# Kernel optimization log

Measured on AMD Instinct MI355X. Metric: run time of the kernel, lower is better.

## Reference

```python
import jax, jax.numpy as jnp
import numpy as np

B, S, D, H = 2, 2048, 1024, 16
DK = D // H


def setup_inputs() -> dict:
    key = jax.random.key(0)
    ks = jax.random.split(key, 8)
    s = 1.0 / np.sqrt(D)
    return {
        "query": jax.random.normal(ks[0], (B, S, D), jnp.float32),
        "key": jax.random.normal(ks[1], (B, S, D), jnp.float32),
        "value": jax.random.normal(ks[2], (B, S, D), jnp.float32),
        "mask": jnp.ones((B, S), jnp.int32),
        "w_q": jax.random.normal(ks[3], (D, D), jnp.float32) * s,
        "w_k": jax.random.normal(ks[4], (D, D), jnp.float32) * s,
        "w_v": jax.random.normal(ks[5], (D, D), jnp.float32) * s,
        "w_o": jax.random.normal(ks[6], (D, D), jnp.float32) * s,
        "b_o": jnp.zeros((D,), jnp.float32),
    }


def reference(query, key, value, mask, w_q, w_k, w_v, w_o, b_o):
    scale = np.sqrt(DK).astype(np.float32)
    # Linear layers: torch stores weight as [out, in], y = x @ W.T
    Q = (query @ w_q.T).reshape(B, S, H, DK).transpose(0, 2, 1, 3)  # [B,H,S,DK]
    K = (key @ w_k.T).reshape(B, S, H, DK).transpose(0, 2, 1, 3)
    V = (value @ w_v.T).reshape(B, S, H, DK).transpose(0, 2, 1, 3)
    scores = jnp.einsum("bhqd,bhkd->bhqk", Q, K) / scale  # [B,H,S,S]
    m = mask[:, None, None, :]  # [B,1,1,S]
    scores = jnp.where(m == 0, jnp.float32(-1e9), scores)
    attn = jax.nn.softmax(scores, axis=-1)  # dropout in eval mode = identity
    ctx = jnp.einsum("bhqk,bhkd->bhqd", attn, V)
    ctx = ctx.transpose(0, 2, 1, 3).reshape(B, S, D)
    out = ctx @ w_o.T + b_o
    return out, attn
```

## Files before the change

### kernel.cpp

```cpp
#include <hip/hip_runtime.h>
#include <hip/hip_bf16.h>
#include <math.h>

#define B 2
#define S 2048
#define D 1024
#define H 16
#define DK 64

typedef __attribute__((ext_vector_type(8))) short bf8;
typedef __attribute__((ext_vector_type(8))) unsigned short u16x8;
typedef __attribute__((ext_vector_type(4))) unsigned short u16x4;
typedef __attribute__((ext_vector_type(4))) float f32x4;
typedef unsigned short ush;

__device__ __forceinline__ float bf2f(ush u) {
    union { unsigned int i; float f; } v; v.i = ((unsigned int)u) << 16; return v.f;
}
__device__ __forceinline__ ush f2bf_rne(float x) {
    __hip_bfloat16 h = __float2bfloat16(x);
    union { __hip_bfloat16 h; ush u; } v; v.h = h; return v.u;
}
__device__ __forceinline__ ush f2bf_trunc(float x) {
    union { float f; unsigned int i; } v; v.f = x; return (ush)(v.i >> 16);
}

__device__ __forceinline__ void gl16(const void* g, void* l) {
    __builtin_amdgcn_global_load_lds(
        (const __attribute__((address_space(1))) void*)g,
        (__attribute__((address_space(3))) void*)l, 16, 0, 0);
}

#define FENCE()    asm volatile("" ::: "memory")
#define WAIT_VM(N) asm volatile("s_waitcnt vmcnt(" #N ")" ::: "memory")
#define BARRAW()   __builtin_amdgcn_s_barrier()

__global__ __launch_bounds__(256) void conv_hex_k(
    const float* __restrict__ q,  ush* __restrict__ qh,  ush* __restrict__ qlo,
    const float* __restrict__ wq, ush* __restrict__ wqh, ush* __restrict__ wql,
    const float* __restrict__ k,  ush* __restrict__ kh,  ush* __restrict__ klo,
    const float* __restrict__ wk, ush* __restrict__ wkh, ush* __restrict__ wkl,
    const float* __restrict__ v,  ush* __restrict__ vh,
    const float* __restrict__ wv, ush* __restrict__ wvh,
    int nbX, int nbW)
{
    int bx = blockIdx.x;
    const float* src; ush* oh; ush* ol;
    if (bx < nbX) { src = q; oh = qh; ol = qlo; }
    else { bx -= nbX;
      if (bx < nbW) { src = wq; oh = wqh; ol = wql; }
      else { bx -= nbW;
        if (bx < nbX) { src = k; oh = kh; ol = klo; }
        else { bx -= nbX;
          if (bx < nbW) { src = wk; oh = wkh; ol = wkl; }
          else { bx -= nbW;
            if (bx < nbX) { src = v; oh = vh; ol = nullptr; }
            else { bx -= nbX; src = wv; oh = wvh; ol = nullptr; }
          } } } }
    const size_t t = (size_t)bx * 256 + threadIdx.x;

    const float4* s4 = (const float4*)src + t * 2;
    float4 a = s4[0], c = s4[1];
    float vv[8] = {a.x, a.y, a.z, a.w, c.x, c.y, c.z, c.w};
    u16x8 hi;
#pragma unroll
    for (int j = 0; j < 8; ++j) hi[j] = f2bf_trunc(vv[j]);
    *(u16x8*)&oh[t * 8] = hi;
    if (ol) {
        u16x8 lo;
#pragma unroll
        for (int j = 0; j < 8; ++j) lo[j] = f2bf_rne(vv[j] - bf2f(hi[j]));
        *(u16x8*)&ol[t * 8] = lo;
    }
}

__global__ __launch_bounds__(256) void conv_hi_k(
    const float* __restrict__ X, ush* __restrict__ Oh)
{
    const size_t t = (size_t)blockIdx.x * 256 + threadIdx.x;
    const float4* s4 = (const float4*)X + t * 2;
    float4 a = s4[0], c = s4[1];
    float v[8] = {a.x, a.y, a.z, a.w, c.x, c.y, c.z, c.w};
    u16x8 hi;
#pragma unroll
    for (int j = 0; j < 8; ++j) hi[j] = f2bf_trunc(v[j]);
    *(u16x8*)&Oh[t * 8] = hi;
}

template<bool SPLIT, int EPI>
__device__ __forceinline__ void gemm_body2(
    const ush* __restrict__ Xh, const ush* __restrict__ Xl,
    const ush* __restrict__ Wh, const ush* __restrict__ Wl,
    const float* __restrict__ bias, void* __restrict__ Y0v, void* __restrict__ Y1v,
    ush* BufS)
{
    const int tid  = threadIdx.x;
    const int lane = tid & 63;
    const int w    = tid >> 6;
    const int wn   = w >> 1, wm = w & 1;
    const int m0   = blockIdx.x * 64;
    const int n0   = blockIdx.y * 128;

    f32x4 acc[4][2];
#pragma unroll
    for (int s = 0; s < 4; ++s)
#pragma unroll
        for (int t = 0; t < 2; ++t) acc[s][t] = (f32x4){0.f, 0.f, 0.f, 0.f};

    const int kg = (lane >> 4) * 8;
    const int rb = lane >> 3;
    const int jd = lane & 7;
    const int kS = SPLIT ? 32 : 16;

    auto stage = [&](ush* buf, int ks) {
#pragma unroll
        for (int i = 0; i < 6; ++i) {
            int rd = w * 48 + i * 8 + rb;
            int jo = jd ^ (rd & 7);
            const ush* src;
            if (rd < 128) {
                if (SPLIT)
                    src = (jo < 4) ? Xh + (size_t)(n0 + rd) * 1024 + ks * 32 + jo * 8
                                   : Xl + (size_t)(n0 + rd) * 1024 + ks * 32 + (jo - 4) * 8;
                else
                    src = Xh + (size_t)(n0 + rd) * 1024 + ks * 64 + jo * 8;
            } else {
                int rw = rd - 128;
                if (SPLIT)
                    src = (jo < 4) ? Wh + (size_t)(m0 + rw) * 1024 + ks * 32 + jo * 8
                                   : Wl + (size_t)(m0 + rw) * 1024 + ks * 32 + (jo - 4) * 8;
                else
                    src = Wh + (size_t)(m0 + rw) * 1024 + ks * 64 + jo * 8;
            }
            gl16(src, &buf[(w * 48 + i * 8) * 64]);
        }
    };

    auto step = [&](const ush* buf) {
        bf8 a0[4], a1[4], b0[2], b1[2];
#pragma unroll
        for (int s = 0; s < 4; ++s) {
            int r = wn * 64 + s * 16 + (lane & 15);
            a0[s] = *(const bf8*)&buf[r * 64 + (kg ^ ((r & 7) << 3))];
            a1[s] = *(const bf8*)&buf[r * 64 + ((32 + kg) ^ ((r & 7) << 3))];
        }
#pragma unroll
        for (int t = 0; t < 2; ++t) {
            int r = wm * 32 + t * 16 + (lane & 15);
            b0[t] = *(const bf8*)&buf[(128 + r) * 64 + (kg ^ ((r & 7) << 3))];
            b1[t] = *(const bf8*)&buf[(128 + r) * 64 + ((32 + kg) ^ ((r & 7) << 3))];
        }
#pragma unroll
        for (int s = 0; s < 4; ++s)
#pragma unroll
            for (int t = 0; t < 2; ++t) {
                acc[s][t] = __builtin_amdgcn_mfma_f32_16x16x32_bf16(a0[s], b0[t], acc[s][t], 0, 0, 0);
                if (SPLIT) {
                    acc[s][t] = __builtin_amdgcn_mfma_f32_16x16x32_bf16(a0[s], b1[t], acc[s][t], 0, 0, 0);
                    acc[s][t] = __builtin_amdgcn_mfma_f32_16x16x32_bf16(a1[s], b0[t], acc[s][t], 0, 0, 0);
                } else {
                    acc[s][t] = __builtin_amdgcn_mfma_f32_16x16x32_bf16(a1[s], b1[t], acc[s][t], 0, 0, 0);
                }
            }
    };

    stage(&BufS[0 * 12288], 0);
    stage(&BufS[1 * 12288], 1);
    FENCE();
    WAIT_VM(6); BARRAW(); FENCE();

    for (int kt = 0; kt < kS; ++kt) {
        const int pf = kt + 2;
        if (pf < kS) { stage(&BufS[(pf % 3) * 12288], pf); FENCE(); }
        step(&BufS[(kt % 3) * 12288]);
        if (kt + 2 < kS)      { WAIT_VM(6); }
        else if (kt + 1 < kS) { WAIT_VM(0); }
        BARRAW(); FENCE();
    }

#pragma unroll
    for (int s = 0; s < 4; ++s)
#pragma unroll
        for (int t = 0; t < 2; ++t) {
            const int nb = n0 + wn * 64 + 16 * s + 4 * (lane >> 4);
            const int m  = m0 + wm * 32 + 16 * t + (lane & 15);
            if (EPI == 0) {
                float* Y = (float*)Y0v;
                const float bb = bias[m];
#pragma unroll
                for (int r = 0; r < 4; ++r)
                    __builtin_nontemporal_store(acc[s][t][r] + bb,
                                                &Y[(size_t)(nb + r) * 1024 + m]);
            } else if (EPI == 1) {
                ush* Yh = (ush*)Y0v;
                ush* Yl = (ush*)Y1v;
#pragma unroll
                for (int r = 0; r < 4; ++r) {
                    float v = acc[s][t][r];
                    ush hi = f2bf_trunc(v);
                    Yh[(size_t)(nb + r) * 1024 + m] = hi;
                    Yl[(size_t)(nb + r) * 1024 + m] = f2bf_rne(v - bf2f(hi));
                }
            } else {
                ush* Vt = (ush*)Y0v;
                u16x4 pk;
#pragma unroll
                for (int r = 0; r < 4; ++r) pk[r] = f2bf_rne(acc[s][t][r]);
                size_t addr = ((size_t)(nb >> 11) * 1024 + m) * 2048 + (nb & 2047);
                *(u16x4*)&Vt[addr] = pk;
            }
        }
}

__global__ __launch_bounds__(256) void gemm_proj3(
    const ush* __restrict__ qXh, const ush* __restrict__ qXl,
    const ush* __restrict__ wqH, const ush* __restrict__ wqL,
    ush* __restrict__ Qh, ush* __restrict__ Ql,
    const ush* __restrict__ kXh, const ush* __restrict__ kXl,
    const ush* __restrict__ wkH, const ush* __restrict__ wkL,
    ush* __restrict__ Kh, ush* __restrict__ Kl,
    const ush* __restrict__ vXh, const ush* __restrict__ wvH,
    ush* __restrict__ Vt)
{
    __shared__ __align__(16) ush BufS[3 * 192 * 64];
    const int z = blockIdx.z;
    if (z == 0)      gemm_body2<true, 1>(qXh, qXl, wqH, wqL, nullptr, Qh, Ql, BufS);
    else if (z == 1) gemm_body2<true, 1>(kXh, kXl, wkH, wkL, nullptr, Kh, Kl, BufS);
    else             gemm_body2<false, 2>(vXh, nullptr, wvH, nullptr, nullptr, Vt, nullptr, BufS);
}

__global__ __launch_bounds__(256) void gemm_outk(
    const ush* __restrict__ Xh, const ush* __restrict__ Wh,
    const float* __restrict__ bias, float* __restrict__ Y)
{
    __shared__ __align__(16) ush BufS[3 * 192 * 64];
    gemm_body2<false, 0>(Xh, nullptr, Wh, nullptr, bias, Y, nullptr, BufS);
}

__global__ __launch_bounds__(512) void attn_mfma4(
    const ush* __restrict__ Qh, const ush* __restrict__ Ql,
    const ush* __restrict__ Kh, const ush* __restrict__ Kl,
    const ush* __restrict__ Vt, const int* __restrict__ maskg,
    float* __restrict__ attn, ush* __restrict__ ctx)
{
    const int tid  = threadIdx.x;
    const int lane = tid & 63;
    const int w    = tid >> 6;
    const int lid  = blockIdx.x + (blockIdx.y << 4) + (blockIdx.z << 8);
    const int swz  = ((lid & 7) << 6) | (lid >> 3);
    const int qt = swz & 15, h = (swz >> 4) & 15, b = swz >> 8;
    const int q0 = qt * 128;

    __shared__ __align__(16) ush KhsD[3][4096];
    __shared__ __align__(16) ush KlsD[2][4096];
    __shared__ __align__(16) ush VtsD[2][4096];
    __shared__ __align__(16) ush Pus[8][1024];
    __shared__ float biasS[2048];

    const int kg = (lane >> 4) * 8;
    const int q  = lane & 15;
    const int qrow = q0 + w * 16 + q;
    const int rb = lane >> 3;
    const int jd = lane & 7;

    const ush* KhT = Kh + (size_t)(b * S) * 1024 + h * DK;
    const ush* KlT = Kl + (size_t)(b * S) * 1024 + h * DK;
    const ush* VtT = Vt + (size_t)(b * 1024 + h * DK) * 2048;

    {
        const int t4 = tid * 4;
        int4 mv = *(const int4*)&maskg[b * S + t4];
        biasS[t4 + 0] = mv.x ? 0.f : -1e9f;
        biasS[t4 + 1] = mv.y ? 0.f : -1e9f;
        biasS[t4 + 2] = mv.z ? 0.f : -1e9f;
        biasS[t4 + 3] = mv.w ? 0.f : -1e9f;
    }

    bf8 qh[2], ql[2];
    {
        const ush* p1 = Qh + (size_t)(b * S + qrow) * D + h * DK + kg;
        qh[0] = *(const bf8*)p1; qh[1] = *(const bf8*)(p1 + 32);
        const ush* p2 = Ql + (size_t)(b * S + qrow) * D + h * DK + kg;
        ql[0] = *(const bf8*)p2; ql[1] = *(const bf8*)(p2 + 32);
    }

    const int rd = w * 8 + rb;
    const int jo = jd ^ (rd & 7);

    auto stKh = [&](int bufi, int k0) {
        gl16(KhT + (size_t)(k0 + rd) * 1024 + jo * 8, &KhsD[bufi][(w * 8) * 64]);
    };
    auto stKl = [&](int bufi, int k0) {
        gl16(KlT + (size_t)(k0 + rd) * 1024 + jo * 8, &KlsD[bufi][(w * 8) * 64]);
    };
    auto stVt = [&](int bufi, int k0) {
        gl16(VtT + (size_t)rd * 2048 + k0 + jo * 8, &VtsD[bufi][(w * 8) * 64]);
    };

    const float scale = 0.125f;
    float mrow = -1e30f, lrow = 0.f;

    auto computeA = [&](const ush* Khs_, int k0) {
        f32x4 sacc[4];
#pragma unroll
        for (int st = 0; st < 4; ++st) sacc[st] = (f32x4){0.f, 0.f, 0.f, 0.f};
#pragma unroll
        for (int st = 0; st < 4; ++st) {
            int r = st * 16 + q;
#pragma unroll
            for (int dh = 0; dh < 2; ++dh) {
                bf8 kf = *(const bf8*)&Khs_[r * 64 + ((dh * 32 + kg) ^ ((r & 7) << 3))];
                sacc[st] = __builtin_amdgcn_mfma_f32_16x16x32_bf16(kf, qh[dh], sacc[st], 0, 0, 0);
            }
        }
        f32x4 bias_r[4];
#pragma unroll
        for (int st = 0; st < 4; ++st)
            bias_r[st] = *(const f32x4*)&biasS[k0 + st * 16 + (lane >> 4) * 4];
        float tmax = -1e30f;
#pragma unroll
        for (int st = 0; st < 4; ++st)
#pragma unroll
            for (int rr = 0; rr < 4; ++rr)
                tmax = fmaxf(tmax, sacc[st][rr] * scale + bias_r[st][rr]);
        tmax = fmaxf(tmax, __shfl_xor(tmax, 16));
        tmax = fmaxf(tmax, __shfl_xor(tmax, 32));
        const float nm = fmaxf(mrow, tmax);
        float ts = 0.f;
#pragma unroll
        for (int st = 0; st < 4; ++st)
#pragma unroll
            for (int rr = 0; rr < 4; ++rr)
                ts += __expf(sacc[st][rr] * scale + bias_r[st][rr] - nm);
        ts += __shfl_xor(ts, 16);
        ts += __shfl_xor(ts, 32);
        lrow = lrow * __expf(mrow - nm) + ts;
        mrow = nm;
    };

    stKh(0, 0); stKh(1, 64);
    __syncthreads();
    {
        int cur = 0, nxt = 2;
        for (int kt = 0; kt < 32; ++kt) {
            if (kt + 2 < 32) stKh(nxt, (kt + 2) * 64);
            FENCE();
            computeA(&KhsD[cur][0], kt * 64);
            if (kt < 30) { WAIT_VM(1); } else { WAIT_VM(0); }
            BARRAW(); FENCE();
            cur = (cur == 2) ? 0 : cur + 1;
            nxt = (nxt == 2) ? 0 : nxt + 1;
        }
    }
    const float inv_l = 1.f / lrow;

    f32x4 cacc[4];
#pragma unroll
    for (int dt = 0; dt < 4; ++dt) cacc[dt] = (f32x4){0.f, 0.f, 0.f, 0.f};
    float* attn_bh = attn + (size_t)(b * H + h) * S * S;

    auto computeB = [&](int bsel, int k0) {
        const ush* Khs_ = &KhsD[bsel][0];
        const ush* Kls_ = &KlsD[bsel][0];
        const ush* Vts_ = &VtsD[bsel][0];
        f32x4 sacc[4];
#pragma unroll
        for (int st = 0; st < 4; ++st) sacc[st] = (f32x4){0.f, 0.f, 0.f, 0.f};
#pragma unroll
        for (int st = 0; st < 4; ++st) {
            int r = st * 16 + q;
#pragma unroll
            for (int dh = 0; dh < 2; ++dh) {
                bf8 kf = *(const bf8*)&Khs_[r * 64 + ((dh * 32 + kg) ^ ((r & 7) << 3))];
                bf8 lf = *(const bf8*)&Kls_[r * 64 + ((dh * 32 + kg) ^ ((r & 7) << 3))];
                sacc[st] = __builtin_amdgcn_mfma_f32_16x16x32_bf16(kf, qh[dh], sacc[st], 0, 0, 0);
                sacc[st] = __builtin_amdgcn_mfma_f32_16x16x32_bf16(kf, ql[dh], sacc[st], 0, 0, 0);
                sacc[st] = __builtin_amdgcn_mfma_f32_16x16x32_bf16(lf, qh[dh], sacc[st], 0, 0, 0);
            }
        }
#pragma unroll
        for (int st = 0; st < 4; ++st) {
            f32x4 bias_r = *(const f32x4*)&biasS[k0 + st * 16 + (lane >> 4) * 4];
            f32x4 pvv;
#pragma unroll
            for (int rr = 0; rr < 4; ++rr)
                pvv[rr] = __expf(sacc[st][rr] * scale + bias_r[rr] - mrow) * inv_l;
            __builtin_nontemporal_store(pvv,
                (f32x4*)&attn_bh[(size_t)(q0 + w * 16 + q) * S + k0 + st * 16 + (lane >> 4) * 4]);
#pragma unroll
            for (int rp = 0; rp < 2; ++rp) {
                int key = st * 16 + (lane >> 4) * 4 + rp * 2;
                unsigned int pk = (unsigned int)f2bf_rne(pvv[rp * 2]) |
                                  ((unsigned int)f2bf_rne(pvv[rp * 2 + 1]) << 16);
                *(unsigned int*)&Pus[w][q * 64 + (key ^ ((q & 7) << 3))] = pk;
            }
        }
        bf8 pa[2];
        pa[0] = *(const bf8*)&Pus[w][q * 64 + ((kg)      ^ ((q & 7) << 3))];
        pa[1] = *(const bf8*)&Pus[w][q * 64 + ((32 + kg) ^ ((q & 7) << 3))];
#pragma unroll
        for (int dt = 0; dt < 4; ++dt) {
            int r = dt * 16 + q;
#pragma unroll
            for (int kc2 = 0; kc2 < 2; ++kc2) {
                bf8 vf = *(const bf8*)&Vts_[r * 64 + ((kc2 * 32 + kg) ^ ((r & 7) << 3))];
                cacc[dt] = __builtin_amdgcn_mfma_f32_16x16x32_bf16(pa[kc2], vf, cacc[dt], 0, 0, 0);
            }
        }
    };

    stKh(0, 0); stKl(0, 0); stVt(0, 0);
    FENCE();
    WAIT_VM(0); BARRAW(); FENCE();
    {
        int cur = 0;
        for (int kt = 0; kt < 32; ++kt) {
            if (kt + 1 < 32) {
                const int kN = (kt + 1) * 64;
                stKh(cur ^ 1, kN); stKl(cur ^ 1, kN); stVt(cur ^ 1, kN);
            }
            FENCE();
            computeB(cur, kt * 64);
            if (kt + 1 < 32) { WAIT_VM(4); } else { FENCE(); }
            BARRAW(); FENCE();
            cur ^= 1;
        }
    }

#pragma unroll
    for (int dt = 0; dt < 4; ++dt)
#pragma unroll
        for (int rr = 0; rr < 4; ++rr) {
            int qq = q0 + w * 16 + 4 * (lane >> 4) + rr;
            ctx[(size_t)(b * S + qq) * D + h * DK + dt * 16 + (lane & 15)] =
                f2bf_rne(cacc[dt][rr]);
        }
}

extern "C" void kernel_launch(void* const* d_in, const int* in_sizes, int n_in,
                              void* d_out, int out_size, void* d_ws, size_t ws_size,
                              hipStream_t stream)
{
    const float* query = (const float*)d_in[0];
    const float* key   = (const float*)d_in[1];
    const float* value = (const float*)d_in[2];
    const int*   mask  = (const int*)d_in[3];
    const float* w_q   = (const float*)d_in[4];
    const float* w_k   = (const float*)d_in[5];
    const float* w_v   = (const float*)d_in[6];
    const float* w_o   = (const float*)d_in[7];
    const float* b_o   = (const float*)d_in[8];

    float* out  = (float*)d_out;
    float* attn = out + (size_t)B * S * D;

    const size_t NE = (size_t)B * S * D;
    const size_t WE = (size_t)D * D;

    ush* Qh = (ush*)d_ws;
    ush* Ql = Qh + NE;
    ush* Kh = Ql + NE;
    ush* Kl = Kh + NE;
    ush* Vt = Kl + NE;
    ush* Cb = Vt + NE;

    ush* qXh = (ush*)attn;
    ush* qXl = qXh + NE;
    ush* kXh = qXl + NE;
    ush* kXl = kXh + NE;
    ush* vXh = kXl + NE;
    ush* wqH = vXh + NE;
    ush* wqL = wqH + WE;
    ush* wkH = wqL + WE;
    ush* wkL = wkH + WE;
    ush* wvH = wkL + WE;
    ush* woH = Qh;

    const dim3 blk(256);
    const dim3 pgrid(D / 64, (B * S) / 128, 3);
    const dim3 ogrid(D / 64, (B * S) / 128);
    const dim3 agrid(S / 128, H, B);

    const int nbX = (int)(NE / 8 / 256);
    const int nbW = (int)(WE / 8 / 256);

    conv_hex_k<<<dim3(3 * nbX + 3 * nbW), blk, 0, stream>>>(
        query, qXh, qXl, w_q, wqH, wqL,
        key,   kXh, kXl, w_k, wkH, wkL,
        value, vXh, w_v, wvH, nbX, nbW);

    gemm_proj3<<<pgrid, blk, 0, stream>>>(
        qXh, qXl, wqH, wqL, Qh, Ql,
        kXh, kXl, wkH, wkL, Kh, Kl,
        vXh, wvH, Vt);

    attn_mfma4<<<agrid, dim3(512), 0, stream>>>(Qh, Ql, Kh, Kl, Vt, mask, attn, Cb);

    conv_hi_k<<<dim3(nbW), blk, 0, stream>>>(w_o, woH);
    gemm_outk<<<ogrid, blk, 0, stream>>>(Cb, woH, b_o, out);
}
```

Baseline: 316.7 us.

## Stage projection epilogues through LDS for coalesced stores; fold w_o conversion into first kernel

```diff
diff --git a/kernel.cpp b/kernel.cpp
--- a/kernel.cpp
+++ b/kernel.cpp
@@ -35,13 +35,14 @@
 #define WAIT_VM(N) asm volatile("s_waitcnt vmcnt(" #N ")" ::: "memory")
 #define BARRAW()   __builtin_amdgcn_s_barrier()
 
-__global__ __launch_bounds__(256) void conv_hex_k(
+__global__ __launch_bounds__(256) void conv_sev_k(
     const float* __restrict__ q,  ush* __restrict__ qh,  ush* __restrict__ qlo,
     const float* __restrict__ wq, ush* __restrict__ wqh, ush* __restrict__ wql,
     const float* __restrict__ k,  ush* __restrict__ kh,  ush* __restrict__ klo,
     const float* __restrict__ wk, ush* __restrict__ wkh, ush* __restrict__ wkl,
     const float* __restrict__ v,  ush* __restrict__ vh,
     const float* __restrict__ wv, ush* __restrict__ wvh,
+    const float* __restrict__ wo, ush* __restrict__ woh,
     int nbX, int nbW)
 {
     int bx = blockIdx.x;
@@ -55,8 +56,10 @@
           if (bx < nbW) { src = wk; oh = wkh; ol = wkl; }
           else { bx -= nbW;
             if (bx < nbX) { src = v; oh = vh; ol = nullptr; }
-            else { bx -= nbX; src = wv; oh = wvh; ol = nullptr; }
-          } } } }
+            else { bx -= nbX;
+              if (bx < nbW) { src = wv; oh = wvh; ol = nullptr; }
+              else { bx -= nbW; src = wo; oh = woh; ol = nullptr; }
+            } } } } }
     const size_t t = (size_t)bx * 256 + threadIdx.x;
 
     const float4* s4 = (const float4*)src + t * 2;
@@ -178,38 +181,73 @@
         BARRAW(); FENCE();
     }
 
-#pragma unroll
-    for (int s = 0; s < 4; ++s)
-#pragma unroll
-        for (int t = 0; t < 2; ++t) {
-            const int nb = n0 + wn * 64 + 16 * s + 4 * (lane >> 4);
-            const int m  = m0 + wm * 32 + 16 * t + (lane & 15);
-            if (EPI == 0) {
+    if (EPI == 0) {
+#pragma unroll
+        for (int s = 0; s < 4; ++s)
+#pragma unroll
+            for (int t = 0; t < 2; ++t) {
+                const int nb = n0 + wn * 64 + 16 * s + 4 * (lane >> 4);
+                const int m  = m0 + wm * 32 + 16 * t + (lane & 15);
                 float* Y = (float*)Y0v;
                 const float bb = bias[m];
 #pragma unroll
                 for (int r = 0; r < 4; ++r)
                     __builtin_nontemporal_store(acc[s][t][r] + bb,
                                                 &Y[(size_t)(nb + r) * 1024 + m]);
-            } else if (EPI == 1) {
-                ush* Yh = (ush*)Y0v;
-                ush* Yl = (ush*)Y1v;
+            }
+    } else if (EPI == 1) {
+        ush* Yt = BufS;
+#pragma unroll
+        for (int pass = 0; pass < 2; ++pass) {
+            __syncthreads();
+#pragma unroll
+            for (int s = 0; s < 4; ++s)
+#pragma unroll
+                for (int t = 0; t < 2; ++t)
+#pragma unroll
+                    for (int r = 0; r < 4; ++r) {
+                        int row = wn * 64 + 16 * s + 4 * (lane >> 4) + r;
+                        int col = wm * 32 + t * 16 + (lane & 15);
+                        float v = acc[s][t][r];
+                        ush hi = f2bf_trunc(v);
+                        ush val = (pass == 0) ? hi : f2bf_rne(v - bf2f(hi));
+                        Yt[row * 64 + (((col >> 3) ^ (row & 7)) * 8 + (col & 7))] = val;
+                    }
+            __syncthreads();
+            ush* Yg = (pass == 0) ? (ush*)Y0v : (ush*)Y1v;
+            const int row = tid >> 1, hh = tid & 1;
+#pragma unroll
+            for (int j = 0; j < 4; ++j) {
+                int c = hh * 4 + j;
+                u16x8 vv = *(const u16x8*)&Yt[row * 64 + ((c ^ (row & 7)) * 8)];
+                *(u16x8*)&Yg[(size_t)(n0 + row) * 1024 + m0 + c * 8] = vv;
+            }
+        }
+    } else {
+        ush* Vl = BufS;
+        __syncthreads();
+#pragma unroll
+        for (int s = 0; s < 4; ++s)
+#pragma unroll
+            for (int t = 0; t < 2; ++t)
 #pragma unroll
                 for (int r = 0; r < 4; ++r) {
-                    float v = acc[s][t][r];
-                    ush hi = f2bf_trunc(v);
-                    Yh[(size_t)(nb + r) * 1024 + m] = hi;
-                    Yl[(size_t)(nb + r) * 1024 + m] = f2bf_rne(v - bf2f(hi));
+                    int sl = wn * 64 + 16 * s + 4 * (lane >> 4) + r;
+                    int ml = wm * 32 + t * 16 + (lane & 15);
+                    Vl[ml * 128 + (((sl >> 3) ^ (ml & 15)) * 8 + (sl & 7))] =
+                        f2bf_rne(acc[s][t][r]);
                 }
-            } else {
-                ush* Vt = (ush*)Y0v;
-                u16x4 pk;
-#pragma unroll
-                for (int r = 0; r < 4; ++r) pk[r] = f2bf_rne(acc[s][t][r]);
-                size_t addr = ((size_t)(nb >> 11) * 1024 + m) * 2048 + (nb & 2047);
-                *(u16x4*)&Vt[addr] = pk;
-            }
-        }
+        __syncthreads();
+        ush* Vt = (ush*)Y0v;
+        const int bq = n0 >> 11;
+        const int ml = tid >> 2, qq = tid & 3;
+#pragma unroll
+        for (int j = 0; j < 4; ++j) {
+            int c = qq * 4 + j;
+            u16x8 vv = *(const u16x8*)&Vl[ml * 128 + ((c ^ (ml & 15)) * 8)];
+            *(u16x8*)&Vt[((size_t)(bq * 1024) + m0 + ml) * 2048 + (n0 & 2047) + c * 8] = vv;
+        }
+    }
 }
 
 __global__ __launch_bounds__(256) void gemm_proj3(
@@ -463,6 +501,9 @@
     ush* Kl = Kh + NE;
     ush* Vt = Kl + NE;
     ush* Cb = Vt + NE;
+    ush* woWS = Cb + NE;
+
+    const bool woInWs = ws_size >= (size_t)(6 * NE + WE) * 2;
 
     ush* qXh = (ush*)attn;
     ush* qXl = qXh + NE;
@@ -474,7 +515,8 @@
     ush* wkH = wqL + WE;
     ush* wkL = wkH + WE;
     ush* wvH = wkL + WE;
-    ush* woH = Qh;
+
+    ush* woH = woInWs ? woWS : Qh;
 
     const dim3 blk(256);
     const dim3 pgrid(D / 64, (B * S) / 128, 3);
@@ -484,10 +526,11 @@
     const int nbX = (int)(NE / 8 / 256);
     const int nbW = (int)(WE / 8 / 256);
 
-    conv_hex_k<<<dim3(3 * nbX + 3 * nbW), blk, 0, stream>>>(
+    const int nseg = 3 * nbX + (woInWs ? 4 : 3) * nbW;
+    conv_sev_k<<<dim3(nseg), blk, 0, stream>>>(
         query, qXh, qXl, w_q, wqH, wqL,
         key,   kXh, kXl, w_k, wkH, wkL,
-        value, vXh, w_v, wvH, nbX, nbW);
+        value, vXh, w_v, wvH, w_o, woH, nbX, nbW);
 
     gemm_proj3<<<pgrid, blk, 0, stream>>>(
         qXh, qXl, wqH, wqL, Qh, Ql,
@@ -496,6 +539,7 @@
 
     attn_mfma4<<<agrid, dim3(512), 0, stream>>>(Qh, Ql, Kh, Kl, Vt, mask, attn, Cb);
 
-    conv_hi_k<<<dim3(nbW), blk, 0, stream>>>(w_o, woH);
+    if (!woInWs)
+        conv_hi_k<<<dim3(nbW), blk, 0, stream>>>(w_o, woH);
     gemm_outk<<<ogrid, blk, 0, stream>>>(Cb, woH, b_o, out);
 }
```

New measurement: 318.2 us. Within noise of the previous version (+0.5%).

## Process two query tiles per attention block and fold w_o conversion into first kernel

Applied to the files above, without the earlier changes.

```diff
diff --git a/kernel.cpp b/kernel.cpp
--- a/kernel.cpp
+++ b/kernel.cpp
@@ -35,13 +35,14 @@
 #define WAIT_VM(N) asm volatile("s_waitcnt vmcnt(" #N ")" ::: "memory")
 #define BARRAW()   __builtin_amdgcn_s_barrier()
 
-__global__ __launch_bounds__(256) void conv_hex_k(
+__global__ __launch_bounds__(256) void conv_sev_k(
     const float* __restrict__ q,  ush* __restrict__ qh,  ush* __restrict__ qlo,
     const float* __restrict__ wq, ush* __restrict__ wqh, ush* __restrict__ wql,
     const float* __restrict__ k,  ush* __restrict__ kh,  ush* __restrict__ klo,
     const float* __restrict__ wk, ush* __restrict__ wkh, ush* __restrict__ wkl,
     const float* __restrict__ v,  ush* __restrict__ vh,
     const float* __restrict__ wv, ush* __restrict__ wvh,
+    const float* __restrict__ wo, ush* __restrict__ woh,
     int nbX, int nbW)
 {
     int bx = blockIdx.x;
@@ -55,8 +56,10 @@
           if (bx < nbW) { src = wk; oh = wkh; ol = wkl; }
           else { bx -= nbW;
             if (bx < nbX) { src = v; oh = vh; ol = nullptr; }
-            else { bx -= nbX; src = wv; oh = wvh; ol = nullptr; }
-          } } } }
+            else { bx -= nbX;
+              if (bx < nbW) { src = wv; oh = wvh; ol = nullptr; }
+              else { bx -= nbW; src = wo; oh = woh; ol = nullptr; }
+            } } } } }
     const size_t t = (size_t)bx * 256 + threadIdx.x;
 
     const float4* s4 = (const float4*)src + t * 2;
@@ -237,7 +240,7 @@
     gemm_body2<false, 0>(Xh, nullptr, Wh, nullptr, bias, Y, nullptr, BufS);
 }
 
-__global__ __launch_bounds__(512) void attn_mfma4(
+__global__ __launch_bounds__(512) void attn_mfma5(
     const ush* __restrict__ Qh, const ush* __restrict__ Ql,
     const ush* __restrict__ Kh, const ush* __restrict__ Kl,
     const ush* __restrict__ Vt, const int* __restrict__ maskg,
@@ -246,10 +249,10 @@
     const int tid  = threadIdx.x;
     const int lane = tid & 63;
     const int w    = tid >> 6;
-    const int lid  = blockIdx.x + (blockIdx.y << 4) + (blockIdx.z << 8);
-    const int swz  = ((lid & 7) << 6) | (lid >> 3);
-    const int qt = swz & 15, h = (swz >> 4) & 15, b = swz >> 8;
-    const int q0 = qt * 128;
+    const int lid  = blockIdx.x + (blockIdx.y << 3) + (blockIdx.z << 7);
+    const int swz  = ((lid & 7) << 5) | (lid >> 3);
+    const int qt = swz & 7, h = (swz >> 3) & 15, b = swz >> 7;
+    const int q0 = qt * 256;
 
     __shared__ __align__(16) ush KhsD[3][4096];
     __shared__ __align__(16) ush KlsD[2][4096];
@@ -259,7 +262,6 @@
 
     const int kg = (lane >> 4) * 8;
     const int q  = lane & 15;
-    const int qrow = q0 + w * 16 + q;
     const int rb = lane >> 3;
     const int jd = lane & 7;
 
@@ -276,12 +278,19 @@
         biasS[t4 + 3] = mv.w ? 0.f : -1e9f;
     }
 
-    bf8 qh[2], ql[2];
+    bf8 qh0[2], ql0[2], qh1[2], ql1[2];
     {
-        const ush* p1 = Qh + (size_t)(b * S + qrow) * D + h * DK + kg;
-        qh[0] = *(const bf8*)p1; qh[1] = *(const bf8*)(p1 + 32);
-        const ush* p2 = Ql + (size_t)(b * S + qrow) * D + h * DK + kg;
-        ql[0] = *(const bf8*)p2; ql[1] = *(const bf8*)(p2 + 32);
+        const int qrow0 = q0 + w * 16 + q;
+        const int qrow1 = q0 + 128 + w * 16 + q;
+        const ush* p;
+        p = Qh + (size_t)(b * S + qrow0) * D + h * DK + kg;
+        qh0[0] = *(const bf8*)p; qh0[1] = *(const bf8*)(p + 32);
+        p = Ql + (size_t)(b * S + qrow0) * D + h * DK + kg;
+        ql0[0] = *(const bf8*)p; ql0[1] = *(const bf8*)(p + 32);
+        p = Qh + (size_t)(b * S + qrow1) * D + h * DK + kg;
+        qh1[0] = *(const bf8*)p; qh1[1] = *(const bf8*)(p + 32);
+        p = Ql + (size_t)(b * S + qrow1) * D + h * DK + kg;
+        ql1[0] = *(const bf8*)p; ql1[1] = *(const bf8*)(p + 32);
     }
 
     const int rd = w * 8 + rb;
@@ -298,9 +307,11 @@
     };
 
     const float scale = 0.125f;
-    float mrow = -1e30f, lrow = 0.f;
-
-    auto computeA = [&](const ush* Khs_, int k0) {
+    float mrow0 = -1e30f, lrow0 = 0.f;
+    float mrow1 = -1e30f, lrow1 = 0.f;
+
+    auto computeA = [&](const ush* Khs_, int k0, const bf8* qhg,
+                        float& mr, float& lr) {
         f32x4 sacc[4];
 #pragma unroll
         for (int st = 0; st < 4; ++st) sacc[st] = (f32x4){0.f, 0.f, 0.f, 0.f};
@@ -310,7 +321,7 @@
 #pragma unroll
             for (int dh = 0; dh < 2; ++dh) {
                 bf8 kf = *(const bf8*)&Khs_[r * 64 + ((dh * 32 + kg) ^ ((r & 7) << 3))];
-                sacc[st] = __builtin_amdgcn_mfma_f32_16x16x32_bf16(kf, qh[dh], sacc[st], 0, 0, 0);
+                sacc[st] = __builtin_amdgcn_mfma_f32_16x16x32_bf16(kf, qhg[dh], sacc[st], 0, 0, 0);
             }
         }
         f32x4 bias_r[4];
@@ -325,7 +336,7 @@
                 tmax = fmaxf(tmax, sacc[st][rr] * scale + bias_r[st][rr]);
         tmax = fmaxf(tmax, __shfl_xor(tmax, 16));
         tmax = fmaxf(tmax, __shfl_xor(tmax, 32));
-        const float nm = fmaxf(mrow, tmax);
+        const float nm = fmaxf(mr, tmax);
         float ts = 0.f;
 #pragma unroll
         for (int st = 0; st < 4; ++st)
@@ -334,8 +345,8 @@
                 ts += __expf(sacc[st][rr] * scale + bias_r[st][rr] - nm);
         ts += __shfl_xor(ts, 16);
         ts += __shfl_xor(ts, 32);
-        lrow = lrow * __expf(mrow - nm) + ts;
-        mrow = nm;
+        lr = lr * __expf(mr - nm) + ts;
+        mr = nm;
     };
 
     stKh(0, 0); stKh(1, 64);
@@ -345,21 +356,28 @@
         for (int kt = 0; kt < 32; ++kt) {
             if (kt + 2 < 32) stKh(nxt, (kt + 2) * 64);
             FENCE();
-            computeA(&KhsD[cur][0], kt * 64);
+            computeA(&KhsD[cur][0], kt * 64, qh0, mrow0, lrow0);
+            computeA(&KhsD[cur][0], kt * 64, qh1, mrow1, lrow1);
             if (kt < 30) { WAIT_VM(1); } else { WAIT_VM(0); }
             BARRAW(); FENCE();
             cur = (cur == 2) ? 0 : cur + 1;
             nxt = (nxt == 2) ? 0 : nxt + 1;
         }
     }
-    const float inv_l = 1.f / lrow;
-
-    f32x4 cacc[4];
-#pragma unroll
-    for (int dt = 0; dt < 4; ++dt) cacc[dt] = (f32x4){0.f, 0.f, 0.f, 0.f};
+    const float inv_l0 = 1.f / lrow0;
+    const float inv_l1 = 1.f / lrow1;
+
+    f32x4 cacc0[4], cacc1[4];
+#pragma unroll
+    for (int dt = 0; dt < 4; ++dt) {
+        cacc0[dt] = (f32x4){0.f, 0.f, 0.f, 0.f};
+        cacc1[dt] = (f32x4){0.f, 0.f, 0.f, 0.f};
+    }
     float* attn_bh = attn + (size_t)(b * H + h) * S * S;
 
-    auto computeB = [&](int bsel, int k0) {
+    auto computeB = [&](int bsel, int k0, int grow,
+                        const bf8* qhg, const bf8* qlg,
+                        float mr, float il, f32x4* caccg) {
         const ush* Khs_ = &KhsD[bsel][0];
         const ush* Kls_ = &KlsD[bsel][0];
         const ush* Vts_ = &VtsD[bsel][0];
@@ -373,9 +391,9 @@
             for (int dh = 0; dh < 2; ++dh) {
                 bf8 kf = *(const bf8*)&Khs_[r * 64 + ((dh * 32 + kg) ^ ((r & 7) << 3))];
                 bf8 lf = *(const bf8*)&Kls_[r * 64 + ((dh * 32 + kg) ^ ((r & 7) << 3))];
-                sacc[st] = __builtin_amdgcn_mfma_f32_16x16x32_bf16(kf, qh[dh], sacc[st], 0, 0, 0);
-                sacc[st] = __builtin_amdgcn_mfma_f32_16x16x32_bf16(kf, ql[dh], sacc[st], 0, 0, 0);
-                sacc[st] = __builtin_amdgcn_mfma_f32_16x16x32_bf16(lf, qh[dh], sacc[st], 0, 0, 0);
+                sacc[st] = __builtin_amdgcn_mfma_f32_16x16x32_bf16(kf, qhg[dh], sacc[st], 0, 0, 0);
+                sacc[st] = __builtin_amdgcn_mfma_f32_16x16x32_bf16(kf, qlg[dh], sacc[st], 0, 0, 0);
+                sacc[st] = __builtin_amdgcn_mfma_f32_16x16x32_bf16(lf, qhg[dh], sacc[st], 0, 0, 0);
             }
         }
 #pragma unroll
@@ -384,9 +402,9 @@
             f32x4 pvv;
 #pragma unroll
             for (int rr = 0; rr < 4; ++rr)
-                pvv[rr] = __expf(sacc[st][rr] * scale + bias_r[rr] - mrow) * inv_l;
+                pvv[rr] = __expf(sacc[st][rr] * scale + bias_r[rr] - mr) * il;
             __builtin_nontemporal_store(pvv,
-                (f32x4*)&attn_bh[(size_t)(q0 + w * 16 + q) * S + k0 + st * 16 + (lane >> 4) * 4]);
+                (f32x4*)&attn_bh[(size_t)(grow + w * 16 + q) * S + k0 + st * 16 + (lane >> 4) * 4]);
 #pragma unroll
             for (int rp = 0; rp < 2; ++rp) {
                 int key = st * 16 + (lane >> 4) * 4 + rp * 2;
@@ -404,7 +422,7 @@
 #pragma unroll
             for (int kc2 = 0; kc2 < 2; ++kc2) {
                 bf8 vf = *(const bf8*)&Vts_[r * 64 + ((kc2 * 32 + kg) ^ ((r & 7) << 3))];
-                cacc[dt] = __builtin_amdgcn_mfma_f32_16x16x32_bf16(pa[kc2], vf, cacc[dt], 0, 0, 0);
+                caccg[dt] = __builtin_amdgcn_mfma_f32_16x16x32_bf16(pa[kc2], vf, caccg[dt], 0, 0, 0);
             }
         }
     };
@@ -420,8 +438,9 @@
                 stKh(cur ^ 1, kN); stKl(cur ^ 1, kN); stVt(cur ^ 1, kN);
             }
             FENCE();
-            computeB(cur, kt * 64);
-            if (kt + 1 < 32) { WAIT_VM(4); } else { FENCE(); }
+            computeB(cur, kt * 64, q0,       qh0, ql0, mrow0, inv_l0, cacc0);
+            computeB(cur, kt * 64, q0 + 128, qh1, ql1, mrow1, inv_l1, cacc1);
+            if (kt + 1 < 32) { WAIT_VM(8); } else { FENCE(); }
             BARRAW(); FENCE();
             cur ^= 1;
         }
@@ -431,9 +450,12 @@
     for (int dt = 0; dt < 4; ++dt)
 #pragma unroll
         for (int rr = 0; rr < 4; ++rr) {
-            int qq = q0 + w * 16 + 4 * (lane >> 4) + rr;
-            ctx[(size_t)(b * S + qq) * D + h * DK + dt * 16 + (lane & 15)] =
-                f2bf_rne(cacc[dt][rr]);
+            int qq0 = q0 + w * 16 + 4 * (lane >> 4) + rr;
+            ctx[(size_t)(b * S + qq0) * D + h * DK + dt * 16 + (lane & 15)] =
+                f2bf_rne(cacc0[dt][rr]);
+            int qq1 = q0 + 128 + w * 16 + 4 * (lane >> 4) + rr;
+            ctx[(size_t)(b * S + qq1) * D + h * DK + dt * 16 + (lane & 15)] =
+                f2bf_rne(cacc1[dt][rr]);
         }
 }
 
@@ -463,6 +485,9 @@
     ush* Kl = Kh + NE;
     ush* Vt = Kl + NE;
     ush* Cb = Vt + NE;
+    ush* woWS = Cb + NE;
+
+    const bool woInWs = ws_size >= (size_t)(6 * NE + WE) * 2;
 
     ush* qXh = (ush*)attn;
     ush* qXl = qXh + NE;
@@ -474,28 +499,31 @@
     ush* wkH = wqL + WE;
     ush* wkL = wkH + WE;
     ush* wvH = wkL + WE;
-    ush* woH = Qh;
+
+    ush* woH = woInWs ? woWS : Qh;
 
     const dim3 blk(256);
     const dim3 pgrid(D / 64, (B * S) / 128, 3);
     const dim3 ogrid(D / 64, (B * S) / 128);
-    const dim3 agrid(S / 128, H, B);
+    const dim3 agrid(S / 256, H, B);
 
     const int nbX = (int)(NE / 8 / 256);
     const int nbW = (int)(WE / 8 / 256);
 
-    conv_hex_k<<<dim3(3 * nbX + 3 * nbW), blk, 0, stream>>>(
+    const int nseg = 3 * nbX + (woInWs ? 4 : 3) * nbW;
+    conv_sev_k<<<dim3(nseg), blk, 0, stream>>>(
         query, qXh, qXl, w_q, wqH, wqL,
         key,   kXh, kXl, w_k, wkH, wkL,
-        value, vXh, w_v, wvH, nbX, nbW);
+        value, vXh, w_v, wvH, w_o, woH, nbX, nbW);
 
     gemm_proj3<<<pgrid, blk, 0, stream>>>(
         qXh, qXl, wqH, wqL, Qh, Ql,
         kXh, kXl, wkH, wkL, Kh, Kl,
         vXh, wvH, Vt);
 
-    attn_mfma4<<<agrid, dim3(512), 0, stream>>>(Qh, Ql, Kh, Kl, Vt, mask, attn, Cb);
-
-    conv_hi_k<<<dim3(nbW), blk, 0, stream>>>(w_o, woH);
+    attn_mfma5<<<agrid, dim3(512), 0, stream>>>(Qh, Ql, Kh, Kl, Vt, mask, attn, Cb);
+
+    if (!woInWs)
+        conv_hi_k<<<dim3(nbW), blk, 0, stream>>>(w_o, woH);
     gemm_outk<<<ogrid, blk, 0, stream>>>(Cb, woH, b_o, out);
 }
```

After: 336.3 us. 1.06x slower.
